# Performance work log

Hardware: AMD Instinct MI355X
Metric: run time of the kernel (lower is better)

## Reference

```python
import jax, jax.numpy as jnp
import numpy as np

HEADS = 12
ROPE_THETA = 10000.0

def _rope(t):
    # t: [B, H, N, D]; lucidrains interleaved RoPE (rotate_half over adjacent pairs)
    B, H, N, D = t.shape
    inv_freq = 1.0 / (ROPE_THETA ** (jnp.arange(0, D, 2, dtype=jnp.float32) / D))  # [D/2]
    freqs = jnp.arange(N, dtype=jnp.float32)[:, None] * inv_freq[None, :]          # [N, D/2]
    freqs = jnp.repeat(freqs, 2, axis=-1)                                          # [N, D]
    cos, sin = jnp.cos(freqs), jnp.sin(freqs)
    tp = t.reshape(B, H, N, D // 2, 2)
    rot = jnp.stack([-tp[..., 1], tp[..., 0]], axis=-1).reshape(B, H, N, D)
    return t * cos + rot * sin

def setup_inputs() -> dict:
    key = jax.random.key(0)
    k1, k2, k3 = jax.random.split(key, 3)
    dim = 768
    x = jax.random.normal(k1, (2, 2048, dim), dtype=jnp.float32)
    w_qkv = jax.random.normal(k2, (3 * dim, dim), dtype=jnp.float32) * (dim ** -0.5)
    w_proj = jax.random.normal(k3, (dim, dim), dtype=jnp.float32) * (dim ** -0.5)
    b_proj = jnp.zeros((dim,), dtype=jnp.float32)
    return {"x": x, "w_qkv": w_qkv, "w_proj": w_proj, "b_proj": b_proj}

def reference(x, w_qkv, w_proj, b_proj):
    B, N, C = x.shape
    H = HEADS
    d = C // H
    scale = d ** -0.5
    qkv = x @ w_qkv.T                                # [B, N, 3C]
    q, k, v = jnp.split(qkv, 3, axis=-1)
    def to_heads(t):
        return t.reshape(B, N, H, d).transpose(0, 2, 1, 3)  # [B,H,N,d]
    q, k, v = map(to_heads, (q, k, v))
    q = _rope(q * scale)
    k = _rope(k)
    attn = jnp.einsum('bhid,bhjd->bhij', q, k)
    attn = jax.nn.softmax(attn, axis=-1)
    out = jnp.einsum('bhij,bhjd->bhid', attn, v)
    out = out.transpose(0, 2, 1, 3).reshape(B, N, C)
    return out @ w_proj.T + b_proj
```

## Files before the change

### kernel.cpp

```cpp
#include <hip/hip_runtime.h>
#include <math.h>

#define NSEQ 2048
#define CDIM 768
#define NH   12
#define HD   64
#define NB   2

typedef unsigned short u16;
typedef __attribute__((ext_vector_type(8))) short bf16x8;
typedef __attribute__((ext_vector_type(4))) float f32x4;
typedef __attribute__((ext_vector_type(8))) float f32x8;
typedef __attribute__((ext_vector_type(4))) __bf16 bf16x4t;
typedef __attribute__((ext_vector_type(8))) __bf16 bf16x8t;

__device__ __forceinline__ u16 f2bf(float x) {
    unsigned int u = __float_as_uint(x);
    u += 0x7fffu + ((u >> 16) & 1u);
    return (u16)(u >> 16);
}

__device__ __forceinline__ uint4 pack8(float4 a, float4 b) {
    f32x8 v = {a.x, a.y, a.z, a.w, b.x, b.y, b.z, b.w};
    union { bf16x8t t; uint4 u; } o;
    o.t = __builtin_convertvector(v, bf16x8t);
    return o.u;
}

#define LSTR 72
#define ESTR 136

#define GLD16(gp, lp) __builtin_amdgcn_global_load_lds( \
    (__attribute__((address_space(1))) void*)(const void*)(gp), \
    (__attribute__((address_space(3))) void*)(void*)(lp), 16, 0, 0)

__global__ __launch_bounds__(256)
void qkv_mfma_kernel(const float* __restrict__ Xf, const float* __restrict__ Wf,
                     u16* __restrict__ Qb, u16* __restrict__ Kb,
                     u16* __restrict__ Vb)
{
    __shared__ __align__(16) u16 S[(128 + 64) * LSTR];
    u16* As = S;
    u16* Bs = S + 128 * LSTR;

    const int tid  = threadIdx.x;
    const int lane = tid & 63;
    const int wid  = tid >> 6;
    const int l15  = lane & 15;
    const int quad = lane >> 4;

    const int f  = blockIdx.x;
    const int L  = (f & 7) * 144 + (f >> 3);
    const int m0 = (L / 36) * 128;
    const int n0 = (L % 36) * 64;

    const int row = tid >> 3, c8s = (tid & 7) << 3;

    f32x4 acc[2][4];
#pragma unroll
    for (int mi = 0; mi < 2; ++mi)
#pragma unroll
        for (int ni = 0; ni < 4; ++ni)
            acc[mi][ni] = (f32x4){0.f, 0.f, 0.f, 0.f};

    float4 pa[4][2], pb[2][2];
#pragma unroll
    for (int it = 0; it < 4; ++it) {
        size_t ga = (size_t)(m0 + row + 32 * it) * CDIM + c8s;
        pa[it][0] = *(const float4*)&Xf[ga];
        pa[it][1] = *(const float4*)&Xf[ga + 4];
    }
#pragma unroll
    for (int it = 0; it < 2; ++it) {
        size_t gb = (size_t)(n0 + row + 32 * it) * CDIM + c8s;
        pb[it][0] = *(const float4*)&Wf[gb];
        pb[it][1] = *(const float4*)&Wf[gb + 4];
    }

    for (int kt = 0; kt < CDIM; kt += 64) {
        __syncthreads();
#pragma unroll
        for (int it = 0; it < 4; ++it)
            *(uint4*)&As[(row + 32 * it) * LSTR + c8s] =
                pack8(pa[it][0], pa[it][1]);
#pragma unroll
        for (int it = 0; it < 2; ++it)
            *(uint4*)&Bs[(row + 32 * it) * LSTR + c8s] =
                pack8(pb[it][0], pb[it][1]);
        __syncthreads();

        if (kt + 64 < CDIM) {
#pragma unroll
            for (int it = 0; it < 4; ++it) {
                size_t ga = (size_t)(m0 + row + 32 * it) * CDIM + kt + 64 + c8s;
                pa[it][0] = *(const float4*)&Xf[ga];
                pa[it][1] = *(const float4*)&Xf[ga + 4];
            }
#pragma unroll
            for (int it = 0; it < 2; ++it) {
                size_t gb = (size_t)(n0 + row + 32 * it) * CDIM + kt + 64 + c8s;
                pb[it][0] = *(const float4*)&Wf[gb];
                pb[it][1] = *(const float4*)&Wf[gb + 4];
            }
        }

#pragma unroll
        for (int k = 0; k < 2; ++k) {
            bf16x8 af[2];
#pragma unroll
            for (int mi = 0; mi < 2; ++mi)
                af[mi] = *(const bf16x8*)
                    &As[(wid * 32 + mi * 16 + l15) * LSTR + quad * 8 + 32 * k];
#pragma unroll
            for (int ni = 0; ni < 4; ++ni) {
                bf16x8 bfr = *(const bf16x8*)
                    &Bs[(ni * 16 + l15) * LSTR + quad * 8 + 32 * k];
#pragma unroll
                for (int mi = 0; mi < 2; ++mi)
                    acc[mi][ni] = __builtin_amdgcn_mfma_f32_16x16x32_bf16(
                        af[mi], bfr, acc[mi][ni], 0, 0, 0);
            }
        }
    }

    __syncthreads();

    const int bi      = m0 >> 11;
    const int tokbase = m0 & 2047;
    const int nbase   = tokbase + wid * 32;
    const int sel     = n0 / CDIM;
    const int h       = (n0 % CDIM) >> 6;

    if (sel == 2) {
        u16* Ew = S;
#pragma unroll
        for (int ni = 0; ni < 4; ++ni)
#pragma unroll
            for (int mi = 0; mi < 2; ++mi)
#pragma unroll
                for (int r = 0; r < 4; ++r)
                    Ew[(ni * 16 + l15) * ESTR + wid * 32 + mi * 16 + quad * 4 + r]
                        = f2bf(acc[mi][ni][r]);
        __syncthreads();
        u16* dst = Vb + (size_t)(bi * NH + h) * HD * NSEQ;
#pragma unroll
        for (int it = 0; it < 4; ++it) {
            int idx = tid + 256 * it;
            int dd  = idx >> 4;
            int c8  = (idx & 15) << 3;
            *(uint4*)&dst[(size_t)dd * NSEQ + tokbase + c8] =
                *(const uint4*)&Ew[dd * ESTR + c8];
        }
    } else {
        u16* dst = ((sel == 0) ? Qb : Kb) + (size_t)(bi * NH + h) * NSEQ * HD;
        const float scl = (sel == 0) ? 0.125f : 1.0f;
        u16* Ew = S + wid * 32 * LSTR;
#pragma unroll
        for (int ni = 0; ni < 4; ++ni) {
            int dd = ni * 16 + l15;
            float invf = expf(-0.14391156831212787f * (float)(dd & ~1));
#pragma unroll
            for (int mi = 0; mi < 2; ++mi) {
                f32x4 val = acc[mi][ni];
#pragma unroll
                for (int r = 0; r < 4; ++r) {
                    float e = val[r] * scl;
                    float p = __shfl_xor(e, 1);
                    int n = nbase + mi * 16 + quad * 4 + r;
                    float sv, cv;
                    __sincosf((float)n * invf, &sv, &cv);
                    float o = (dd & 1) ? (e * cv + p * sv)
                                       : (e * cv - p * sv);
                    Ew[(mi * 16 + quad * 4 + r) * LSTR + dd] = f2bf(o);
                }
            }
        }
#pragma unroll
        for (int it = 0; it < 4; ++it) {
            int ch  = lane + 64 * it;
            int tr  = ch >> 3;
            int gc8 = (ch & 7) << 3;
            *(uint4*)&dst[(size_t)(nbase + tr) * HD + gc8] =
                *(const uint4*)&Ew[tr * LSTR + gc8];
        }
    }
}

#define STAGE_KV(BUF, kt_) do {                                               \
    GLD16(Kg + ((size_t)(((kt_) << 6) + r0) * HD + cs),                       \
          &Ks[BUF][wid * 512]);                                               \
    GLD16(Kg + ((size_t)(((kt_) << 6) + r0 + 32) * HD + cs),                  \
          &Ks[BUF][wid * 512 + 2048]);                                        \
    GLD16(Vg + ((size_t)r0 * NSEQ + ((kt_) << 6) + cs),                       \
          &Vs[BUF][wid * 512]);                                               \
    GLD16(Vg + ((size_t)(r0 + 32) * NSEQ + ((kt_) << 6) + cs),                \
          &Vs[BUF][wid * 512 + 2048]);                                        \
} while (0)

#define ATTN_STEP(kt_, CUR, NXT) do {                                         \
    if ((kt_) + 1 < NSEQ / 64) STAGE_KV(NXT, (kt_) + 1);                      \
    f32x4 sacc[4];                                                            \
    _Pragma("unroll")                                                         \
    for (int mt = 0; mt < 4; ++mt) sacc[mt] = (f32x4){0.f, 0.f, 0.f, 0.f};    \
    _Pragma("unroll")                                                         \
    for (int k = 0; k < 2; ++k) {                                             \
        _Pragma("unroll")                                                     \
        for (int mt = 0; mt < 4; ++mt) {                                      \
            bf16x8 ak = *(const bf16x8*)                                      \
                &Ks[CUR][(mt * 16 + l15) * 64 + ((quad * 8 + 32 * k) ^ swz)]; \
            sacc[mt] = __builtin_amdgcn_mfma_f32_16x16x32_bf16(               \
                ak, aq[k], sacc[mt], 0, 0, 0);                                \
        }                                                                     \
    }                                                                         \
    _Pragma("unroll")                                                         \
    for (int mt = 0; mt < 4; ++mt) {                                          \
        f32x4 ev;                                                             \
        _Pragma("unroll")                                                     \
        for (int r = 0; r < 4; ++r) ev[r] = __expf(sacc[mt][r]);              \
        bf16x4t pbk = __builtin_convertvector(ev, bf16x4t);                   \
        *(bf16x4t*)&Pw[l15 * 64 + ((mt * 16 + quad * 4) ^ swz)] = pbk;        \
    }                                                                         \
    _Pragma("unroll")                                                         \
    for (int k = 0; k < 2; ++k) {                                             \
        bf16x8 ap = *(const bf16x8*)                                          \
            &Pw[l15 * 64 + ((quad * 8 + 32 * k) ^ swz)];                      \
        lacc = __builtin_amdgcn_mfma_f32_16x16x32_bf16(                       \
            ap, vone, lacc, 0, 0, 0);                                         \
        _Pragma("unroll")                                                     \
        for (int t = 0; t < 4; ++t) {                                         \
            bf16x8 bv = *(const bf16x8*)                                      \
                &Vs[CUR][(t * 16 + l15) * 64 + ((quad * 8 + 32 * k) ^ swz)];  \
            O[t] = __builtin_amdgcn_mfma_f32_16x16x32_bf16(                   \
                ap, bv, O[t], 0, 0, 0);                                       \
        }                                                                     \
    }                                                                         \
    __syncthreads();                                                          \
} while (0)

__global__ __launch_bounds__(256)
void attn_kernel(const u16* __restrict__ Qb, const u16* __restrict__ Kb,
                 const u16* __restrict__ Vt, u16* __restrict__ AO)
{
    __shared__ __align__(16) u16 Ks[2][64 * 64];
    __shared__ __align__(16) u16 Vs[2][64 * 64];
    __shared__ __align__(16) u16 Ps[4][16 * 64];

    const int tid  = threadIdx.x;
    const int lane = tid & 63;
    const int wid  = tid >> 6;
    const int l15  = lane & 15;
    const int quad = lane >> 4;
    const int swz  = (l15 & 7) << 3;

    const int f  = blockIdx.x;
    const int i  = f >> 3;
    const int bh = (f & 7) * 3 + (i >> 5);
    const int qt = i & 31;

    const u16* Qg = Qb + ((size_t)bh * NSEQ + qt * 64) * HD;
    const u16* Kg = Kb + (size_t)bh * NSEQ * HD;
    const u16* Vg = Vt + (size_t)bh * HD * NSEQ;

    const int r0 = tid >> 3;
    const int cs = ((tid & 7) ^ (r0 & 7)) << 3;

    bf16x8 aq[2];
    aq[0] = *(const bf16x8*)&Qg[(wid * 16 + l15) * HD + quad * 8];
    aq[1] = *(const bf16x8*)&Qg[(wid * 16 + l15) * HD + quad * 8 + 32];

    union { u16 s[8]; bf16x8 v; } oneu;
#pragma unroll
    for (int ii = 0; ii < 8; ++ii) oneu.s[ii] = 0x3f80;
    const bf16x8 vone = oneu.v;

    f32x4 O[4];
#pragma unroll
    for (int t = 0; t < 4; ++t) O[t] = (f32x4){0.f, 0.f, 0.f, 0.f};
    f32x4 lacc = (f32x4){0.f, 0.f, 0.f, 0.f};

    u16* Pw = Ps[wid];

    STAGE_KV(0, 0);
    __syncthreads();

    for (int kt = 0; kt < NSEQ / 64; kt += 2) {
        ATTN_STEP(kt, 0, 1);
        ATTN_STEP(kt + 1, 1, 0);
    }

    float inv4[4];
#pragma unroll
    for (int r = 0; r < 4; ++r) inv4[r] = 1.0f / lacc[r];

    const int b = bh / NH, h = bh % NH;
#pragma unroll
    for (int r = 0; r < 4; ++r) {
        size_t orow = (size_t)b * NSEQ + qt * 64 + wid * 16 + quad * 4 + r;
#pragma unroll
        for (int t = 0; t < 4; ++t)
            AO[orow * CDIM + h * HD + t * 16 + l15] = f2bf(O[t][r] * inv4[r]);
    }
}

__global__ __launch_bounds__(256)
void proj_kernel(const u16* __restrict__ A, const float* __restrict__ Wf,
                 const float* __restrict__ bias, float* __restrict__ out)
{
    __shared__ __align__(16) u16 As[64 * 64];
    __shared__ __align__(16) u16 Bs[64 * 64];
    const int tid  = threadIdx.x;
    const int lane = tid & 63;
    const int wid  = tid >> 6;
    const int l15  = lane & 15;
    const int quad = lane >> 4;
    const int swz  = (l15 & 7) << 3;
    const int wr = wid >> 1, wc = wid & 1;
    const int m0 = blockIdx.x * 64;
    const int n0 = blockIdx.y * 64;

    const int r0 = tid >> 3;
    const int cs = ((tid & 7) ^ (r0 & 7)) << 3;
    const int c8 = (tid & 7) << 3;
    const int bswz = c8 ^ ((r0 & 7) << 3);

    f32x4 acc[2][2];
#pragma unroll
    for (int mi = 0; mi < 2; ++mi)
#pragma unroll
        for (int ni = 0; ni < 2; ++ni)
            acc[mi][ni] = (f32x4){0.f, 0.f, 0.f, 0.f};

    for (int kt = 0; kt < CDIM; kt += 64) {
        __syncthreads();
        GLD16(A + ((size_t)(m0 + r0) * CDIM + kt + cs),      &As[wid * 512]);
        GLD16(A + ((size_t)(m0 + r0 + 32) * CDIM + kt + cs), &As[wid * 512 + 2048]);
        {
            size_t gb0 = (size_t)(n0 + r0) * CDIM + kt + c8;
            size_t gb1 = (size_t)(n0 + r0 + 32) * CDIM + kt + c8;
            float4 w0 = *(const float4*)&Wf[gb0];
            float4 w1 = *(const float4*)&Wf[gb0 + 4];
            float4 w2 = *(const float4*)&Wf[gb1];
            float4 w3 = *(const float4*)&Wf[gb1 + 4];
            *(uint4*)&Bs[r0 * 64 + bswz]        = pack8(w0, w1);
            *(uint4*)&Bs[(r0 + 32) * 64 + bswz] = pack8(w2, w3);
        }
        __syncthreads();

#pragma unroll
        for (int k = 0; k < 2; ++k) {
            bf16x8 af[2], bf[2];
#pragma unroll
            for (int mi = 0; mi < 2; ++mi)
                af[mi] = *(const bf16x8*)
                    &As[(wr * 32 + mi * 16 + l15) * 64 + ((quad * 8 + 32 * k) ^ swz)];
#pragma unroll
            for (int ni = 0; ni < 2; ++ni)
                bf[ni] = *(const bf16x8*)
                    &Bs[(wc * 32 + ni * 16 + l15) * 64 + ((quad * 8 + 32 * k) ^ swz)];
#pragma unroll
            for (int mi = 0; mi < 2; ++mi)
#pragma unroll
                for (int ni = 0; ni < 2; ++ni)
                    acc[mi][ni] = __builtin_amdgcn_mfma_f32_16x16x32_bf16(
                        af[mi], bf[ni], acc[mi][ni], 0, 0, 0);
        }
    }

#pragma unroll
    for (int ni = 0; ni < 2; ++ni) {
        int col = n0 + wc * 32 + ni * 16 + l15;
        float bb = bias[col];
#pragma unroll
        for (int mi = 0; mi < 2; ++mi) {
            int rw = m0 + wr * 32 + mi * 16 + quad * 4;
#pragma unroll
            for (int r = 0; r < 4; ++r)
                out[(size_t)(rw + r) * CDIM + col] = acc[mi][ni][r] + bb;
        }
    }
}

extern "C" void kernel_launch(void* const* d_in, const int* in_sizes, int n_in,
                              void* d_out, int out_size, void* d_ws,
                              size_t ws_size, hipStream_t stream)
{
    const float* X     = (const float*)d_in[0];
    const float* Wqkv  = (const float*)d_in[1];
    const float* Wproj = (const float*)d_in[2];
    const float* bias  = (const float*)d_in[3];
    float* out = (float*)d_out;

    const size_t per_buf = (size_t)NB * NH * NSEQ * HD;
    u16* Qb  = (u16*)d_ws;
    u16* Kb  = Qb + per_buf;
    u16* Vb  = Kb + per_buf;
    u16* AOb = Vb + per_buf;

    qkv_mfma_kernel<<<dim3(1152), 256, 0, stream>>>(X, Wqkv, Qb, Kb, Vb);
    attn_kernel<<<dim3(768), 256, 0, stream>>>(Qb, Kb, Vb, AOb);
    proj_kernel<<<dim3(64, 12), 256, 0, stream>>>(AOb, Wproj, bias, out);
}
```

Baseline: 162.2 us.

## Pre-convert inputs to bf16 and double-buffer GEMM tiles via direct LDS loads

Adds a conversion kernel that casts X, Wqkv (with the 0.125 query scale folded into the Q rows of the weights) and Wproj to bf16 once per call. The QKV and projection GEMMs then load bf16 tiles straight into XOR-swizzled, double-buffered LDS using global_load_lds, prefetching the next k-tile while computing the current one. Block-to-tile mapping is also reshuffled for cache locality. The cost is an extra kernel launch and an extra pass over inputs and weights, in exchange for half the GEMM global traffic and no in-loop fp32-to-bf16 packing.

```diff
diff --git a/kernel.cpp b/kernel.cpp
--- a/kernel.cpp
+++ b/kernel.cpp
@@ -35,26 +35,58 @@
     (__attribute__((address_space(3))) void*)(void*)(lp), 16, 0, 0)
 
 __global__ __launch_bounds__(256)
-void qkv_mfma_kernel(const float* __restrict__ Xf, const float* __restrict__ Wf,
+void conv_kernel(const float* __restrict__ Xf, const float* __restrict__ Wqkv,
+                 const float* __restrict__ Wproj, u16* __restrict__ Xb,
+                 u16* __restrict__ Wqb, u16* __restrict__ Wpb)
+{
+    const int c = blockIdx.x * 256 + threadIdx.x;
+    const float* src; u16* dst; int lc; float scl = 1.0f;
+    if (c < 393216)      { src = Xf;    dst = Xb;  lc = c; }
+    else if (c < 614400) { src = Wqkv;  dst = Wqb; lc = c - 393216;
+                           if (lc < 73728) scl = 0.125f; }
+    else                 { src = Wproj; dst = Wpb; lc = c - 614400; }
+    float4 a = *(const float4*)&src[(size_t)lc * 8];
+    float4 b = *(const float4*)&src[(size_t)lc * 8 + 4];
+    a.x *= scl; a.y *= scl; a.z *= scl; a.w *= scl;
+    b.x *= scl; b.y *= scl; b.z *= scl; b.w *= scl;
+    *(uint4*)&dst[(size_t)lc * 8] = pack8(a, b);
+}
+
+#define QKV_STAGE(BUF, kt_) do {                                              \
+    _Pragma("unroll")                                                         \
+    for (int it = 0; it < 4; ++it) {                                          \
+        int ch = tid + 256 * it; int rr = ch >> 3;                            \
+        int sc = ((ch & 7) ^ (rr & 7)) << 3;                                  \
+        GLD16(Xg + (size_t)(m0 + rr) * CDIM + (kt_) + sc, &S[BUF][ch * 8]);   \
+    }                                                                         \
+    _Pragma("unroll")                                                         \
+    for (int it = 0; it < 2; ++it) {                                          \
+        int ch = tid + 256 * it; int rr = ch >> 3;                            \
+        int sc = ((ch & 7) ^ (rr & 7)) << 3;                                  \
+        GLD16(Wg + (size_t)(n0 + rr) * CDIM + (kt_) + sc,                     \
+              &S[BUF][8192 + ch * 8]);                                        \
+    }                                                                         \
+} while (0)
+
+__global__ __launch_bounds__(256)
+void qkv_mfma_kernel(const u16* __restrict__ Xg, const u16* __restrict__ Wg,
                      u16* __restrict__ Qb, u16* __restrict__ Kb,
                      u16* __restrict__ Vb)
 {
-    __shared__ __align__(16) u16 S[(128 + 64) * LSTR];
-    u16* As = S;
-    u16* Bs = S + 128 * LSTR;
+    __shared__ __align__(16) u16 S[2][12288];
 
     const int tid  = threadIdx.x;
     const int lane = tid & 63;
     const int wid  = tid >> 6;
     const int l15  = lane & 15;
     const int quad = lane >> 4;
+    const int swz  = (l15 & 7) << 3;
 
     const int f  = blockIdx.x;
-    const int L  = (f & 7) * 144 + (f >> 3);
-    const int m0 = (L / 36) * 128;
-    const int n0 = (L % 36) * 64;
-
-    const int row = tid >> 3, c8s = (tid & 7) << 3;
+    const int xc = f & 7;
+    const int s  = f >> 3;
+    const int m0 = (xc * 4 + (s & 3)) * 128;
+    const int n0 = (s >> 2) * 64;
 
     f32x4 acc[2][4];
 #pragma unroll
@@ -63,46 +95,12 @@
         for (int ni = 0; ni < 4; ++ni)
             acc[mi][ni] = (f32x4){0.f, 0.f, 0.f, 0.f};
 
-    float4 pa[4][2], pb[2][2];
-#pragma unroll
-    for (int it = 0; it < 4; ++it) {
-        size_t ga = (size_t)(m0 + row + 32 * it) * CDIM + c8s;
-        pa[it][0] = *(const float4*)&Xf[ga];
-        pa[it][1] = *(const float4*)&Xf[ga + 4];
-    }
-#pragma unroll
-    for (int it = 0; it < 2; ++it) {
-        size_t gb = (size_t)(n0 + row + 32 * it) * CDIM + c8s;
-        pb[it][0] = *(const float4*)&Wf[gb];
-        pb[it][1] = *(const float4*)&Wf[gb + 4];
-    }
-
+    QKV_STAGE(0, 0);
+    __syncthreads();
+
+    int cur = 0;
     for (int kt = 0; kt < CDIM; kt += 64) {
-        __syncthreads();
-#pragma unroll
-        for (int it = 0; it < 4; ++it)
-            *(uint4*)&As[(row + 32 * it) * LSTR + c8s] =
-                pack8(pa[it][0], pa[it][1]);
-#pragma unroll
-        for (int it = 0; it < 2; ++it)
-            *(uint4*)&Bs[(row + 32 * it) * LSTR + c8s] =
-                pack8(pb[it][0], pb[it][1]);
-        __syncthreads();
-
-        if (kt + 64 < CDIM) {
-#pragma unroll
-            for (int it = 0; it < 4; ++it) {
-                size_t ga = (size_t)(m0 + row + 32 * it) * CDIM + kt + 64 + c8s;
-                pa[it][0] = *(const float4*)&Xf[ga];
-                pa[it][1] = *(const float4*)&Xf[ga + 4];
-            }
-#pragma unroll
-            for (int it = 0; it < 2; ++it) {
-                size_t gb = (size_t)(n0 + row + 32 * it) * CDIM + kt + 64 + c8s;
-                pb[it][0] = *(const float4*)&Wf[gb];
-                pb[it][1] = *(const float4*)&Wf[gb + 4];
-            }
-        }
+        if (kt + 64 < CDIM) QKV_STAGE(cur ^ 1, kt + 64);
 
 #pragma unroll
         for (int k = 0; k < 2; ++k) {
@@ -110,29 +108,32 @@
 #pragma unroll
             for (int mi = 0; mi < 2; ++mi)
                 af[mi] = *(const bf16x8*)
-                    &As[(wid * 32 + mi * 16 + l15) * LSTR + quad * 8 + 32 * k];
+                    &S[cur][(wid * 32 + mi * 16 + l15) * 64
+                            + ((quad * 8 + 32 * k) ^ swz)];
 #pragma unroll
             for (int ni = 0; ni < 4; ++ni) {
                 bf16x8 bfr = *(const bf16x8*)
-                    &Bs[(ni * 16 + l15) * LSTR + quad * 8 + 32 * k];
+                    &S[cur][8192 + (ni * 16 + l15) * 64
+                            + ((quad * 8 + 32 * k) ^ swz)];
 #pragma unroll
                 for (int mi = 0; mi < 2; ++mi)
                     acc[mi][ni] = __builtin_amdgcn_mfma_f32_16x16x32_bf16(
                         af[mi], bfr, acc[mi][ni], 0, 0, 0);
             }
         }
-    }
-
-    __syncthreads();
+        __syncthreads();
+        cur ^= 1;
+    }
 
     const int bi      = m0 >> 11;
     const int tokbase = m0 & 2047;
     const int nbase   = tokbase + wid * 32;
     const int sel     = n0 / CDIM;
     const int h       = (n0 % CDIM) >> 6;
+    u16* Sf = &S[0][0];
 
     if (sel == 2) {
-        u16* Ew = S;
+        u16* Ew = Sf;
 #pragma unroll
         for (int ni = 0; ni < 4; ++ni)
 #pragma unroll
@@ -153,8 +154,7 @@
         }
     } else {
         u16* dst = ((sel == 0) ? Qb : Kb) + (size_t)(bi * NH + h) * NSEQ * HD;
-        const float scl = (sel == 0) ? 0.125f : 1.0f;
-        u16* Ew = S + wid * 32 * LSTR;
+        u16* Ew = Sf + wid * 32 * LSTR;
 #pragma unroll
         for (int ni = 0; ni < 4; ++ni) {
             int dd = ni * 16 + l15;
@@ -164,7 +164,7 @@
                 f32x4 val = acc[mi][ni];
 #pragma unroll
                 for (int r = 0; r < 4; ++r) {
-                    float e = val[r] * scl;
+                    float e = val[r];
                     float p = __shfl_xor(e, 1);
                     int n = nbase + mi * 16 + quad * 4 + r;
                     float sv, cv;
@@ -302,12 +302,22 @@
     }
 }
 
+#define PROJ_STAGE(BUF, kt_) do {                                             \
+    _Pragma("unroll")                                                         \
+    for (int it = 0; it < 2; ++it) {                                          \
+        int ch = tid + 256 * it; int rr = ch >> 3;                            \
+        int sc = ((ch & 7) ^ (rr & 7)) << 3;                                  \
+        GLD16(Ag + (size_t)(m0 + rr) * CDIM + (kt_) + sc, &S[BUF][ch * 8]);   \
+        GLD16(Wg + (size_t)(n0 + rr) * CDIM + (kt_) + sc,                     \
+              &S[BUF][4096 + ch * 8]);                                        \
+    }                                                                         \
+} while (0)
+
 __global__ __launch_bounds__(256)
-void proj_kernel(const u16* __restrict__ A, const float* __restrict__ Wf,
+void proj_kernel(const u16* __restrict__ Ag, const u16* __restrict__ Wg,
                  const float* __restrict__ bias, float* __restrict__ out)
 {
-    __shared__ __align__(16) u16 As[64 * 64];
-    __shared__ __align__(16) u16 Bs[64 * 64];
+    __shared__ __align__(16) u16 S[2][8192];
     const int tid  = threadIdx.x;
     const int lane = tid & 63;
     const int wid  = tid >> 6;
@@ -315,13 +325,12 @@
     const int quad = lane >> 4;
     const int swz  = (l15 & 7) << 3;
     const int wr = wid >> 1, wc = wid & 1;
-    const int m0 = blockIdx.x * 64;
-    const int n0 = blockIdx.y * 64;
-
-    const int r0 = tid >> 3;
-    const int cs = ((tid & 7) ^ (r0 & 7)) << 3;
-    const int c8 = (tid & 7) << 3;
-    const int bswz = c8 ^ ((r0 & 7) << 3);
+
+    const int f  = blockIdx.x;
+    const int xc = f & 7;
+    const int s  = f >> 3;
+    const int m0 = (xc * 8 + (s & 7)) * 64;
+    const int n0 = (s >> 3) * 64;
 
     f32x4 acc[2][2];
 #pragma unroll
@@ -330,21 +339,12 @@
         for (int ni = 0; ni < 2; ++ni)
             acc[mi][ni] = (f32x4){0.f, 0.f, 0.f, 0.f};
 
+    PROJ_STAGE(0, 0);
+    __syncthreads();
+
+    int cur = 0;
     for (int kt = 0; kt < CDIM; kt += 64) {
-        __syncthreads();
-        GLD16(A + ((size_t)(m0 + r0) * CDIM + kt + cs),      &As[wid * 512]);
-        GLD16(A + ((size_t)(m0 + r0 + 32) * CDIM + kt + cs), &As[wid * 512 + 2048]);
-        {
-            size_t gb0 = (size_t)(n0 + r0) * CDIM + kt + c8;
-            size_t gb1 = (size_t)(n0 + r0 + 32) * CDIM + kt + c8;
-            float4 w0 = *(const float4*)&Wf[gb0];
-            float4 w1 = *(const float4*)&Wf[gb0 + 4];
-            float4 w2 = *(const float4*)&Wf[gb1];
-            float4 w3 = *(const float4*)&Wf[gb1 + 4];
-            *(uint4*)&Bs[r0 * 64 + bswz]        = pack8(w0, w1);
-            *(uint4*)&Bs[(r0 + 32) * 64 + bswz] = pack8(w2, w3);
-        }
-        __syncthreads();
+        if (kt + 64 < CDIM) PROJ_STAGE(cur ^ 1, kt + 64);
 
 #pragma unroll
         for (int k = 0; k < 2; ++k) {
@@ -352,11 +352,13 @@
 #pragma unroll
             for (int mi = 0; mi < 2; ++mi)
                 af[mi] = *(const bf16x8*)
-                    &As[(wr * 32 + mi * 16 + l15) * 64 + ((quad * 8 + 32 * k) ^ swz)];
+                    &S[cur][(wr * 32 + mi * 16 + l15) * 64
+                            + ((quad * 8 + 32 * k) ^ swz)];
 #pragma unroll
             for (int ni = 0; ni < 2; ++ni)
                 bf[ni] = *(const bf16x8*)
-                    &Bs[(wc * 32 + ni * 16 + l15) * 64 + ((quad * 8 + 32 * k) ^ swz)];
+                    &S[cur][4096 + (wc * 32 + ni * 16 + l15) * 64
+                            + ((quad * 8 + 32 * k) ^ swz)];
 #pragma unroll
             for (int mi = 0; mi < 2; ++mi)
 #pragma unroll
@@ -364,6 +366,8 @@
                     acc[mi][ni] = __builtin_amdgcn_mfma_f32_16x16x32_bf16(
                         af[mi], bf[ni], acc[mi][ni], 0, 0, 0);
         }
+        __syncthreads();
+        cur ^= 1;
     }
 
 #pragma unroll
@@ -394,9 +398,12 @@
     u16* Qb  = (u16*)d_ws;
     u16* Kb  = Qb + per_buf;
     u16* Vb  = Kb + per_buf;
-    u16* AOb = Vb + per_buf;
-
-    qkv_mfma_kernel<<<dim3(1152), 256, 0, stream>>>(X, Wqkv, Qb, Kb, Vb);
-    attn_kernel<<<dim3(768), 256, 0, stream>>>(Qb, Kb, Vb, AOb);
-    proj_kernel<<<dim3(64, 12), 256, 0, stream>>>(AOb, Wproj, bias, out);
-}
+    u16* XAO = Vb + per_buf;
+    u16* Wqb = XAO + per_buf;
+    u16* Wpb = Wqb + (size_t)3 * CDIM * CDIM;
+
+    conv_kernel<<<dim3(2688), 256, 0, stream>>>(X, Wqkv, Wproj, XAO, Wqb, Wpb);
+    qkv_mfma_kernel<<<dim3(1152), 256, 0, stream>>>(XAO, Wqb, Qb, Kb, Vb);
+    attn_kernel<<<dim3(768), 256, 0, stream>>>(Qb, Kb, Vb, XAO);
+    proj_kernel<<<dim3(768), 256, 0, stream>>>(XAO, Wpb, bias, out);
+}
```

After: 147.8 us. -8.8%, faster.
